# Kernel optimization log

Measured on AMD Instinct MI355X. Metric: run time of the kernel, lower is better.

## Reference

```python
import jax, jax.numpy as jnp
import numpy as np

N_NODES = 50000
N_EDGES = 1600000
D_IN = 128
D_HID = 256   # 2 * input_dims
FC1 = 256
FC2 = 256
N_ACT = 8
EPS = 1e-5


def layer_norm(x, w, b):
    mu = jnp.mean(x, axis=-1, keepdims=True)
    var = jnp.mean((x - mu) ** 2, axis=-1, keepdims=True)
    return (x - mu) * jax.lax.rsqrt(var + EPS) * w + b


def setup_inputs() -> dict:
    key = jax.random.key(0)
    ks = jax.random.split(key, 16)
    state = jax.random.normal(ks[0], (N_NODES, D_IN), dtype=jnp.float32)
    edge_index = jax.random.randint(ks[1], (2, N_EDGES), 0, N_NODES, dtype=jnp.int64)
    agent_i = 7
    # GCNConv params (glorot-ish init is fine for a numeric reference)
    conv_w = jax.random.normal(ks[2], (D_IN, D_HID), dtype=jnp.float32) / np.sqrt(D_IN)
    conv_b = jnp.zeros((D_HID,), dtype=jnp.float32)
    f1 = 1.0 / np.sqrt(D_HID)
    fc1_w = jax.random.uniform(ks[3], (D_HID, FC1), minval=-f1, maxval=f1, dtype=jnp.float32)
    fc1_b = jax.random.uniform(ks[4], (FC1,), minval=-f1, maxval=f1, dtype=jnp.float32)
    f2 = 1.0 / np.sqrt(FC1)
    fc2_w = jax.random.uniform(ks[5], (FC1, FC2), minval=-f2, maxval=f2, dtype=jnp.float32)
    fc2_b = jax.random.uniform(ks[6], (FC2,), minval=-f2, maxval=f2, dtype=jnp.float32)
    ln1_w = jnp.ones((FC1,), dtype=jnp.float32)
    ln1_b = jnp.zeros((FC1,), dtype=jnp.float32)
    ln2_w = jnp.ones((FC2,), dtype=jnp.float32)
    ln2_b = jnp.zeros((FC2,), dtype=jnp.float32)
    f3 = 0.003
    mu_w = jax.random.uniform(ks[7], (FC2, N_ACT), minval=-f3, maxval=f3, dtype=jnp.float32)
    mu_b = jax.random.uniform(ks[8], (N_ACT,), minval=-f3, maxval=f3, dtype=jnp.float32)
    return {
        "state": state, "edge_index": edge_index, "agent_i": agent_i,
        "conv_w": conv_w, "conv_b": conv_b,
        "fc1_w": fc1_w, "fc1_b": fc1_b, "ln1_w": ln1_w, "ln1_b": ln1_b,
        "fc2_w": fc2_w, "fc2_b": fc2_b, "ln2_w": ln2_w, "ln2_b": ln2_b,
        "mu_w": mu_w, "mu_b": mu_b,
    }


def gcn_conv(x, edge_index, w, b):
    N = x.shape[0]
    loops = jnp.arange(N, dtype=edge_index.dtype)
    src = jnp.concatenate([edge_index[0], loops])
    dst = jnp.concatenate([edge_index[1], loops])
    ones = jnp.ones(src.shape[0], dtype=x.dtype)
    deg = jax.ops.segment_sum(ones, dst, num_segments=N)
    dinv = jnp.where(deg > 0, jax.lax.rsqrt(deg), 0.0)
    norm = dinv[src] * dinv[dst]                        # [E+N]
    h = x @ w                                           # [N, D_HID]
    msg = h[src] * norm[:, None]                        # gather: [E+N, D_HID]
    return jax.ops.segment_sum(msg, dst, num_segments=N) + b


def reference(state, edge_index, agent_i, conv_w, conv_b,
              fc1_w, fc1_b, ln1_w, ln1_b, fc2_w, fc2_b, ln2_w, ln2_b,
              mu_w, mu_b):
    x = gcn_conv(state, edge_index, conv_w, conv_b)     # [N, D_HID]
    x = jax.nn.relu(x[agent_i])                         # [D_HID]
    x = jax.nn.relu(layer_norm(x @ fc1_w + fc1_b, ln1_w, ln1_b))
    x = jax.nn.relu(layer_norm(x @ fc2_w + fc2_b, ln2_w, ln2_b))
    return jax.nn.sigmoid(x @ mu_w + mu_b)              # [N_ACT]
```

## Files before the change

kernel.cpp:

```cpp
#include <hip/hip_runtime.h>
#include <hip/hip_bf16.h>

#define D_IN  128
#define D_HID 256
#define NB_A  256
#define NT_A  512
#define NB_B  256
#define NT_B  512
#define NT_C  512
#define MAXG  512
#define HASHN 2048
#define PBM_STRIDE 72

#define OFF_BAR  0
#define OFF_M    16
#define OFF_DEG  32
#define OFF_PBM  1024
#define OFF_CM   20480
#define OFF_MAP  21504
#define OFF_H0   24576
#define OFF_H1   25088
#define OFF_H2   25600

#define ALD(p)   __hip_atomic_load((p),      __ATOMIC_RELAXED, __HIP_MEMORY_SCOPE_AGENT)
#define AST(p,v) __hip_atomic_store((p),(v), __ATOMIC_RELAXED, __HIP_MEMORY_SCOPE_AGENT)

__device__ __forceinline__ float ldf(const void* p, long long i, bool b16) {
    if (b16) {
        unsigned short u = ((const unsigned short*)p)[i];
        return __uint_as_float(((unsigned int)u) << 16);
    }
    return ((const float*)p)[i];
}

__device__ __forceinline__ unsigned hash_n(int key) {
    return (((unsigned)key * 2654435761u) >> 21) & (HASHN - 1);
}

__device__ __forceinline__ int detect_i64(const void* edges, int tid, int* s) {
    if (tid < 64) {
        const unsigned* w = (const unsigned*)edges;
        unsigned long long b = __ballot(w[2 * tid + 1] == 0u);
        if (tid == 0) *s = (b == ~0ULL) ? 1 : 0;
    }
    __syncthreads();
    return *s;
}

__device__ __forceinline__ int detect_b16(const void* state, int tid, int* s) {
    if (tid < 64) {
        const unsigned short* p = (const unsigned short*)state;
        unsigned short v = p[tid];
        int e = (v >> 7) & 0xff;
        unsigned long long b = __ballot(v == 0 || (e >= 90 && e <= 140));
        if (tid == 0) *s = (b == ~0ULL) ? 1 : 0;
    }
    __syncthreads();
    return *s;
}

__device__ __forceinline__ void bar_arrive(int* slot) {
    __syncthreads();
    if (threadIdx.x == 0) {
        __threadfence();
        __hip_atomic_fetch_add(slot, 1, __ATOMIC_RELEASE, __HIP_MEMORY_SCOPE_AGENT);
    }
}

__device__ __forceinline__ void bar_wait(int* slot, int cnt) {
    if (threadIdx.x == 0) {
        while (__hip_atomic_load(slot, __ATOMIC_RELAXED, __HIP_MEMORY_SCOPE_AGENT) < cnt)
            __builtin_amdgcn_s_sleep(2);
        __threadfence();
    }
    __syncthreads();
}

__global__ void __launch_bounds__(NT_A) k_A(const void* edges, const void* state,
                                            const int* agent_p,
                                            const void* w0, const void* w1,
                                            const void* w2, const void* w3,
                                            int* wsi, long long n_edges) {
    __shared__ int s_pref[NT_A];
    __shared__ int s_list[64];
    __shared__ int s_i64, s_b16;
    int tid = threadIdx.x, bid = blockIdx.x;
    int i64 = detect_i64(edges, tid, &s_i64);
    int b16 = detect_b16(state, tid, &s_b16);

    if (bid == 0) {
        if (tid < 8) AST(&wsi[OFF_BAR + tid], 0);
        for (int i = tid; i <= MAXG; i += NT_A) AST(&wsi[OFF_DEG + i], 0);
    }

    {
        int esz = b16 ? 2 : 4;
        long long gt = (long long)bid * NT_A + tid;
        const void* arr[4] = { w0, w1, w2, w3 };
        const int elems[4] = { D_IN * D_HID, D_HID * D_HID, D_HID * D_HID, D_HID * 8 };
        long long base = 0;
        #pragma unroll
        for (int a = 0; a < 4; a++) {
            long long lines = ((long long)elems[a] * esz) >> 6;
            long long idx = gt - base;
            if (idx >= 0 && idx < lines) {
                unsigned v = *(const unsigned*)((const char*)arr[a] + (idx << 6));
                asm volatile("" :: "v"(v));
            }
            base += lines;
        }
    }

    int agent = agent_p[0];
    long long base8 = ((long long)bid * NT_A + tid) * 8;
    const long long stride8 = (long long)NB_A * NT_A * 8;
    long long nv = n_edges & ~7LL;
    int c = 0;
    if (i64) {
        const long long* dst = (const long long*)edges + n_edges;
        for (long long e = base8; e < nv; e += stride8) {
            long2 a0 = *(const long2*)(dst + e);
            long2 a1 = *(const long2*)(dst + e + 2);
            long2 a2 = *(const long2*)(dst + e + 4);
            long2 a3 = *(const long2*)(dst + e + 6);
            c += ((int)a0.x == agent) + ((int)a0.y == agent)
               + ((int)a1.x == agent) + ((int)a1.y == agent)
               + ((int)a2.x == agent) + ((int)a2.y == agent)
               + ((int)a3.x == agent) + ((int)a3.y == agent);
        }
        if (bid == 0 && tid == 0)
            for (long long e = nv; e < n_edges; e++) c += ((int)dst[e] == agent);
    } else {
        const int* dst = (const int*)edges + n_edges;
        for (long long e = base8; e < nv; e += stride8) {
            int4 a = *(const int4*)(dst + e);
            int4 b = *(const int4*)(dst + e + 4);
            c += (a.x == agent) + (a.y == agent) + (a.z == agent) + (a.w == agent)
               + (b.x == agent) + (b.y == agent) + (b.z == agent) + (b.w == agent);
        }
        if (bid == 0 && tid == 0)
            for (long long e = nv; e < n_edges; e++) c += (dst[e] == agent);
    }
    s_pref[tid] = c;
    __syncthreads();
    #pragma unroll
    for (int off = 1; off < NT_A; off <<= 1) {
        int v = (tid >= off) ? s_pref[tid - off] : 0;
        __syncthreads();
        s_pref[tid] += v;
        __syncthreads();
    }
    int excl = s_pref[tid] - c;
    int total = s_pref[NT_A - 1];
    if (c > 0 && excl < 64) {
        int k = excl;
        if (i64) {
            const long long* src = (const long long*)edges;
            const long long* dst = src + n_edges;
            for (long long e = base8; e < nv; e += stride8) {
                #pragma unroll
                for (int q = 0; q < 8; q++) {
                    if ((int)dst[e + q] == agent) { if (k < 64) s_list[k] = (int)src[e + q]; k++; }
                }
            }
            if (bid == 0 && tid == 0)
                for (long long e = nv; e < n_edges; e++)
                    if ((int)dst[e] == agent) { if (k < 64) s_list[k] = (int)src[e]; k++; }
        } else {
            const int* src = (const int*)edges;
            const int* dst = src + n_edges;
            for (long long e = base8; e < nv; e += stride8) {
                #pragma unroll
                for (int q = 0; q < 8; q++) {
                    if (dst[e + q] == agent) { if (k < 64) s_list[k] = src[e + q]; k++; }
                }
            }
            if (bid == 0 && tid == 0)
                for (long long e = nv; e < n_edges; e++)
                    if (dst[e] == agent) { if (k < 64) s_list[k] = src[e]; k++; }
        }
    }
    __syncthreads();
    int* reg = wsi + OFF_PBM + bid * PBM_STRIDE;
    int tw = total < 64 ? total : 64;
    if (tid == 0) reg[0] = tw;
    if (tid < tw) reg[1 + tid] = s_list[tid];
}

__global__ void __launch_bounds__(NT_B) k_B(const void* edges, const int* agent_p,
                                            int* wsi, long long n_edges) {
    __shared__ int s_pref[NT_B];
    __shared__ int s_nodes[MAXG + 1];
    __shared__ int s_hkey[HASHN];
    __shared__ int s_hval[HASHN];
    __shared__ int s_cnt[MAXG + 1];
    __shared__ int s_i64, s_nu;
    int tid = threadIdx.x, bid = blockIdx.x;
    int i64 = detect_i64(edges, tid, &s_i64);

    int bc = 0;
    if (tid < NB_A) {
        bc = wsi[OFF_PBM + tid * PBM_STRIDE];
        bc = bc < 64 ? (bc < 0 ? 0 : bc) : 64;
    }
    s_pref[tid] = bc;
    __syncthreads();
    #pragma unroll
    for (int off = 1; off < NT_B; off <<= 1) {
        int v = (tid >= off) ? s_pref[tid - off] : 0;
        __syncthreads();
        s_pref[tid] += v;
        __syncthreads();
    }
    int excl = s_pref[tid] - bc;
    int mc = s_pref[NT_B - 1];
    int m = mc < MAXG ? mc : MAXG;
    if (tid < NB_A) {
        for (int i = 0; i < bc; i++) {
            int g = excl + i;
            if (g < MAXG) s_nodes[1 + g] = wsi[OFF_PBM + tid * PBM_STRIDE + 1 + i];
        }
    }
    if (tid == 0) s_nodes[0] = agent_p[0];
    for (int i = tid; i < HASHN; i += NT_B) s_hkey[i] = -1;
    for (int i = tid; i <= m; i += NT_B) s_cnt[i] = 0;
    __syncthreads();

    if (tid == 0) {
        int nu = 0;
        for (int j = 0; j <= m; j++) {
            int key = s_nodes[j];
            unsigned h = hash_n(key);
            while (true) {
                if (s_hkey[h] == -1) { s_hkey[h] = key; s_hval[h] = nu++; break; }
                if (s_hkey[h] == key) break;
                h = (h + 1) & (HASHN - 1);
            }
        }
        s_nu = nu;
    }
    __syncthreads();

    auto probe = [&](int d) {
        unsigned h = hash_n(d);
        while (true) {
            int k = s_hkey[h];
            if (k == -1) break;
            if (k == d) { atomicAdd(&s_cnt[s_hval[h]], 1); break; }
            h = (h + 1) & (HASHN - 1);
        }
    };

    long long base8 = ((long long)bid * NT_B + tid) * 8;
    const long long stride8 = (long long)NB_B * NT_B * 8;
    long long nv = n_edges & ~7LL;
    if (i64) {
        const long long* dst = (const long long*)edges + n_edges;
        for (long long e = base8; e < nv; e += stride8) {
            long2 a0 = *(const long2*)(dst + e);
            long2 a1 = *(const long2*)(dst + e + 2);
            long2 a2 = *(const long2*)(dst + e + 4);
            long2 a3 = *(const long2*)(dst + e + 6);
            probe((int)a0.x); probe((int)a0.y); probe((int)a1.x); probe((int)a1.y);
            probe((int)a2.x); probe((int)a2.y); probe((int)a3.x); probe((int)a3.y);
        }
        if (bid == 0 && tid == 0)
            for (long long e = nv; e < n_edges; e++) probe((int)dst[e]);
    } else {
        const int* dst = (const int*)edges + n_edges;
        for (long long e = base8; e < nv; e += stride8) {
            int4 a = *(const int4*)(dst + e);
            int4 b = *(const int4*)(dst + e + 4);
            probe(a.x); probe(a.y); probe(a.z); probe(a.w);
            probe(b.x); probe(b.y); probe(b.z); probe(b.w);
        }
        if (bid == 0 && tid == 0)
            for (long long e = nv; e < n_edges; e++) probe(dst[e]);
    }
    __syncthreads();
    int nu = s_nu;
    for (int i = tid; i < nu; i += NT_B)
        if (s_cnt[i]) atomicAdd(&wsi[OFF_DEG + i], s_cnt[i]);
    if (bid == 0) {
        if (tid == 0) wsi[OFF_M] = m;
        for (int i = tid; i < m; i += NT_B) wsi[OFF_CM + i] = s_nodes[1 + i];
        for (int j = tid; j <= m; j += NT_B) {
            int key = s_nodes[j];
            unsigned h = hash_n(key);
            while (s_hkey[h] != key) h = (h + 1) & (HASHN - 1);
            wsi[OFF_MAP + j] = s_hval[h];
        }
    }
}

__device__ __forceinline__ float ln256(float v, const void* lnw, const void* lnb,
                                       float* s_red, int tid, bool b16) {
    if (tid < 256) {
        float x = v;
        #pragma unroll
        for (int o = 32; o > 0; o >>= 1) x += __shfl_down(x, o);
        if ((tid & 63) == 0) s_red[tid >> 6] = x;
    }
    __syncthreads();
    float mu = (s_red[0] + s_red[1] + s_red[2] + s_red[3]) * (1.0f / 256.0f);
    if (tid < 256) {
        float dd = v - mu;
        float x = dd * dd;
        #pragma unroll
        for (int o = 32; o > 0; o >>= 1) x += __shfl_down(x, o);
        if ((tid & 63) == 0) s_red[4 + (tid >> 6)] = x;
    }
    __syncthreads();
    float var = (s_red[4] + s_red[5] + s_red[6] + s_red[7]) * (1.0f / 256.0f);
    float y = 0.0f;
    if (tid < 256)
        y = fmaxf((v - mu) * rsqrtf(var + 1e-5f) * ldf(lnw, tid, b16) + ldf(lnb, tid, b16), 0.0f);
    __syncthreads();
    return y;
}

__global__ void __launch_bounds__(NT_C) k_C(
    const void* state, const int* agent_p,
    const void* conv_w, const void* conv_b,
    const void* fc1_w, const void* fc1_b, const void* ln1_w, const void* ln1_b,
    const void* fc2_w, const void* fc2_b, const void* ln2_w, const void* ln2_b,
    const void* mu_w, const void* mu_b,
    int* wsi, void* out)
{
    __shared__ float s_wl[8192];
    __shared__ float s_in[D_HID];
    __shared__ float s_part[NT_C];
    __shared__ float s_xs[D_IN];
    __shared__ float s_red[8];
    __shared__ int   s_src[MAXG];
    __shared__ float s_w[MAXG];
    __shared__ int   s_b16;

    int tid = threadIdx.x, bid = blockIdx.x;
    bool b16 = detect_b16(state, tid, &s_b16) != 0;
    float* wsf = (float*)wsi;
    int* bar = wsi + OFF_BAR;

    if (bid < 8) {
        int o0 = bid * 32;
        for (int i = tid; i < D_IN * 32; i += NT_C)
            s_wl[i] = ldf(conv_w, (long long)(i >> 5) * D_HID + o0 + (i & 31), b16);
    } else if (bid < 16) {
        int o0 = (bid - 8) * 32;
        for (int i = tid; i < D_HID * 32; i += NT_C)
            s_wl[i] = ldf(fc1_w, (long long)(i >> 5) * D_HID + o0 + (i & 31), b16);
    } else if (bid < 24) {
        int o0 = (bid - 16) * 32;
        for (int i = tid; i < D_HID * 32; i += NT_C)
            s_wl[i] = ldf(fc2_w, (long long)(i >> 5) * D_HID + o0 + (i & 31), b16);
    } else {
        for (int i = tid; i < D_HID * 8; i += NT_C)
            s_wl[i] = ldf(mu_w, i, b16);
    }

    if (bid < 8) {
        int m = wsi[OFF_M];
        m = m < MAXG ? m : MAXG;
        int agent = agent_p[0];
        float dinv_a = rsqrtf((float)(ALD(&wsi[OFF_DEG]) + 1));
        for (int i = tid; i < m; i += NT_C) {
            s_src[i] = wsi[OFF_CM + i];
            int u = wsi[OFF_MAP + 1 + i];
            s_w[i] = dinv_a * rsqrtf((float)(ALD(&wsi[OFF_DEG + u]) + 1));
        }
        __syncthreads();
        int d = tid & 127, jg = tid >> 7;
        float acc = (jg == 0) ? dinv_a * dinv_a * ldf(state, (long long)agent * D_IN + d, b16) : 0.0f;
        for (int j = jg; j < m; j += 4)
            acc += s_w[j] * ldf(state, (long long)s_src[j] * D_IN + d, b16);
        s_part[tid] = acc;
        __syncthreads();
        if (tid < D_IN)
            s_xs[tid] = s_part[tid] + s_part[tid + 128] + s_part[tid + 256] + s_part[tid + 384];
        __syncthreads();
        int c = tid & 31, ks = tid >> 5;
        float a = 0.0f;
        #pragma unroll 8
        for (int k = ks * 8; k < ks * 8 + 8; k++)
            a += s_xs[k] * s_wl[k * 32 + c];
        s_part[tid] = a;
        __syncthreads();
        if (tid < 32) {
            int oo = bid * 32 + tid;
            float h = ldf(conv_b, oo, b16);
            #pragma unroll
            for (int s2 = 0; s2 < 16; s2++) h += s_part[s2 * 32 + tid];
            AST(&wsf[OFF_H0 + oo], fmaxf(h, 0.0f));
        }
        bar_arrive(&bar[0]);
        return;
    }

    if (bid < 16) {
        bar_wait(&bar[0], 8);
        if (tid < D_HID) s_in[tid] = ALD(&wsf[OFF_H0 + tid]);
        __syncthreads();
        int c = tid & 31, ks = tid >> 5;
        float a = 0.0f;
        #pragma unroll 8
        for (int k = ks * 16; k < ks * 16 + 16; k++)
            a += s_in[k] * s_wl[k * 32 + c];
        s_part[tid] = a;
        __syncthreads();
        if (tid < 32) {
            int oo = (bid - 8) * 32 + tid;
            float h = ldf(fc1_b, oo, b16);
            #pragma unroll
            for (int s2 = 0; s2 < 16; s2++) h += s_part[s2 * 32 + tid];
            AST(&wsf[OFF_H1 + oo], h);
        }
        bar_arrive(&bar[1]);
        return;
    }

    if (bid < 24) {
        bar_wait(&bar[1], 8);
        float v = (tid < D_HID) ? ALD(&wsf[OFF_H1 + tid]) : 0.0f;
        float y = ln256(v, ln1_w, ln1_b, s_red, tid, b16);
        if (tid < D_HID) s_in[tid] = y;
        __syncthreads();
        int c = tid & 31, ks = tid >> 5;
        float a = 0.0f;
        #pragma unroll 8
        for (int k = ks * 16; k < ks * 16 + 16; k++)
            a += s_in[k] * s_wl[k * 32 + c];
        s_part[tid] = a;
        __syncthreads();
        if (tid < 32) {
            int oo = (bid - 16) * 32 + tid;
            float h = ldf(fc2_b, oo, b16);
            #pragma unroll
            for (int s2 = 0; s2 < 16; s2++) h += s_part[s2 * 32 + tid];
            AST(&wsf[OFF_H2 + oo], h);
        }
        bar_arrive(&bar[2]);
        return;
    }

    {
        bar_wait(&bar[2], 8);
        float v = (tid < D_HID) ? ALD(&wsf[OFF_H2 + tid]) : 0.0f;
        float y = ln256(v, ln2_w, ln2_b, s_red, tid, b16);
        if (tid < D_HID) s_in[tid] = y;
        __syncthreads();
        int o = tid & 7, ks = tid >> 3;
        float a = 0.0f;
        #pragma unroll
        for (int k = ks * 4; k < ks * 4 + 4; k++)
            a += s_in[k] * s_wl[k * 8 + o];
        s_part[tid] = a;
        __syncthreads();
        if (tid < 8) {
            float acc = ldf(mu_b, tid, b16);
            #pragma unroll
            for (int s2 = 0; s2 < 64; s2++) acc += s_part[s2 * 8 + tid];
            float r = 1.0f / (1.0f + expf(-acc));
            if (b16) ((__hip_bfloat16*)out)[tid] = __float2bfloat16(r);
            else     ((float*)out)[tid] = r;
        }
    }
}

extern "C" void kernel_launch(void* const* d_in, const int* in_sizes, int n_in,
                              void* d_out, int out_size, void* d_ws, size_t ws_size,
                              hipStream_t stream) {
    const void* state = d_in[0];
    const void* edges = d_in[1];
    const int* agent = (const int*)d_in[2];
    int* wsi = (int*)d_ws;
    long long n_edges = in_sizes[1] / 2;

    k_A<<<NB_A, NT_A, 0, stream>>>(edges, state, agent,
                                   d_in[3], d_in[5], d_in[9], d_in[13],
                                   wsi, n_edges);
    k_B<<<NB_B, NT_B, 0, stream>>>(edges, agent, wsi, n_edges);
    k_C<<<25, NT_C, 0, stream>>>(state, agent,
                                 d_in[3], d_in[4],
                                 d_in[5], d_in[6], d_in[7], d_in[8],
                                 d_in[9], d_in[10], d_in[11], d_in[12],
                                 d_in[13], d_in[14],
                                 wsi, d_out);
}
```

Baseline: 35.96 us.

## Prefetch neighbor state rows into cache in k_B and vectorize k_C gather

In k_B, the first 8 blocks touch each gathered neighbor's state row (one load per 64-byte chunk) so those rows are cache-resident when k_C runs its gather. The k_C aggregation now loads two features per thread via float2/packed bf16 and splits neighbors across 8 groups instead of 4, reducing serial load latency per thread. This adds extra memory traffic and work to k_B blocks, and relies on the rows staying in L2 between kernel launches.

```diff
diff --git a/kernel.cpp b/kernel.cpp
--- a/kernel.cpp
+++ b/kernel.cpp
@@ -31,6 +31,17 @@
         return __uint_as_float(((unsigned int)u) << 16);
     }
     return ((const float*)p)[i];
+}
+
+__device__ __forceinline__ void ld2(const void* p, long long i, bool b16, float& a, float& b) {
+    if (b16) {
+        unsigned int u = ((const unsigned int*)p)[i >> 1];
+        a = __uint_as_float(u << 16);
+        b = __uint_as_float(u & 0xffff0000u);
+    } else {
+        float2 v = ((const float2*)p)[i >> 1];
+        a = v.x; b = v.y;
+    }
 }
 
 __device__ __forceinline__ unsigned hash_n(int key) {
@@ -187,16 +198,18 @@
     if (tid < tw) reg[1 + tid] = s_list[tid];
 }
 
-__global__ void __launch_bounds__(NT_B) k_B(const void* edges, const int* agent_p,
+__global__ void __launch_bounds__(NT_B) k_B(const void* edges, const void* state,
+                                            const int* agent_p,
                                             int* wsi, long long n_edges) {
     __shared__ int s_pref[NT_B];
     __shared__ int s_nodes[MAXG + 1];
     __shared__ int s_hkey[HASHN];
     __shared__ int s_hval[HASHN];
     __shared__ int s_cnt[MAXG + 1];
-    __shared__ int s_i64, s_nu;
+    __shared__ int s_i64, s_b16, s_nu;
     int tid = threadIdx.x, bid = blockIdx.x;
     int i64 = detect_i64(edges, tid, &s_i64);
+    bool b16 = detect_b16(state, tid, &s_b16) != 0;
 
     int bc = 0;
     if (tid < NB_A) {
@@ -240,6 +253,17 @@
         s_nu = nu;
     }
     __syncthreads();
+
+    if (bid < 8) {
+        int esz = b16 ? 2 : 4;
+        int chunks = (D_IN * esz) >> 6;
+        for (int i = tid; i < (m + 1) * chunks; i += NT_B) {
+            int j = i / chunks, ch = i - j * chunks;
+            long long row = s_nodes[j];
+            unsigned v = *(const unsigned*)((const char*)state + row * D_IN * esz + ch * 64);
+            asm volatile("" :: "v"(v));
+        }
+    }
 
     auto probe = [&](int d) {
         unsigned h = hash_n(d);
@@ -328,6 +352,7 @@
     int* wsi, void* out)
 {
     __shared__ float s_wl[8192];
+    __shared__ float s_g[1024];
     __shared__ float s_in[D_HID];
     __shared__ float s_part[NT_C];
     __shared__ float s_xs[D_IN];
@@ -369,14 +394,31 @@
             s_w[i] = dinv_a * rsqrtf((float)(ALD(&wsi[OFF_DEG + u]) + 1));
         }
         __syncthreads();
-        int d = tid & 127, jg = tid >> 7;
-        float acc = (jg == 0) ? dinv_a * dinv_a * ldf(state, (long long)agent * D_IN + d, b16) : 0.0f;
-        for (int j = jg; j < m; j += 4)
-            acc += s_w[j] * ldf(state, (long long)s_src[j] * D_IN + d, b16);
-        s_part[tid] = acc;
-        __syncthreads();
-        if (tid < D_IN)
-            s_xs[tid] = s_part[tid] + s_part[tid + 128] + s_part[tid + 256] + s_part[tid + 384];
+        int jg = tid >> 6;
+        int d2 = (tid & 63) * 2;
+        float a0 = 0.0f, a1 = 0.0f;
+        if (jg == 0) {
+            float sa, sb;
+            ld2(state, (long long)agent * D_IN + d2, b16, sa, sb);
+            a0 = dinv_a * dinv_a * sa;
+            a1 = dinv_a * dinv_a * sb;
+        }
+        for (int j = jg; j < m; j += 8) {
+            float sa, sb;
+            ld2(state, (long long)s_src[j] * D_IN + d2, b16, sa, sb);
+            float w = s_w[j];
+            a0 += w * sa;
+            a1 += w * sb;
+        }
+        s_g[jg * 128 + d2]     = a0;
+        s_g[jg * 128 + d2 + 1] = a1;
+        __syncthreads();
+        if (tid < D_IN) {
+            float acc = 0.0f;
+            #pragma unroll
+            for (int g = 0; g < 8; g++) acc += s_g[g * 128 + tid];
+            s_xs[tid] = acc;
+        }
         __syncthreads();
         int c = tid & 31, ks = tid >> 5;
         float a = 0.0f;
@@ -478,7 +520,7 @@
     k_A<<<NB_A, NT_A, 0, stream>>>(edges, state, agent,
                                    d_in[3], d_in[5], d_in[9], d_in[13],
                                    wsi, n_edges);
-    k_B<<<NB_B, NT_B, 0, stream>>>(edges, agent, wsi, n_edges);
+    k_B<<<NB_B, NT_B, 0, stream>>>(edges, state, agent, wsi, n_edges);
     k_C<<<25, NT_C, 0, stream>>>(state, agent,
                                  d_in[3], d_in[4],
                                  d_in[5], d_in[6], d_in[7], d_in[8],
```

Measured after the change: 34.04 us. 5.3% less time.
